# Kernel tuning notes

Hardware: AMD Instinct MI355X
Metric: run time of the kernel (lower is better)

## Reference

```python
import jax, jax.numpy as jnp
import numpy as np

D_MODEL = 1024
N_HEADS = 16
D_HEAD = D_MODEL // N_HEADS


def setup_inputs() -> dict:
    key = jax.random.key(0)
    k1, k2, k3 = jax.random.split(key, 3)
    B, T = 2, 2048
    x = jax.random.normal(k1, (B, T, D_MODEL), dtype=jnp.float32)
    key_padding_mask = jnp.zeros((B, T), dtype=bool)  # True = padded key
    # nn.Linear weights: [out_features, in_features], bias=False
    W_qkv = jax.random.normal(k2, (3 * D_MODEL, D_MODEL), dtype=jnp.float32) * (D_MODEL ** -0.5)
    W_proj = jax.random.normal(k3, (D_MODEL, D_MODEL), dtype=jnp.float32) * (D_MODEL ** -0.5)
    return {"x": x, "key_padding_mask": key_padding_mask, "W_qkv": W_qkv, "W_proj": W_proj}


def reference(x, key_padding_mask, W_qkv, W_proj):
    B, T, D = x.shape
    H, Dh = N_HEADS, D_HEAD
    scale = Dh ** -0.5
    # qkv: [B,T,3D] -> [3,B,H,T,Dh]
    qkv = (x @ W_qkv.T).reshape(B, T, 3, H, Dh).transpose(2, 0, 3, 1, 4)
    q, k, v = qkv[0], qkv[1], qkv[2]
    # attention scores [B,H,T,T]
    attn = jnp.einsum("bhqd,bhkd->bhqk", q, k) * scale
    attn = jnp.where(key_padding_mask[:, None, None, :], -jnp.inf, attn)
    attn = jax.nn.softmax(attn, axis=-1)  # dropout in eval mode = identity
    out = jnp.einsum("bhqk,bhkd->bhqd", attn, v)
    out = out.transpose(0, 2, 1, 3).reshape(B, T, D)
    return out @ W_proj.T
```

## Files before the change

### kernel.cpp

```cpp
#include <hip/hip_runtime.h>
#include <hip/hip_bf16.h>

typedef unsigned short u16;
typedef unsigned int u32;
typedef __bf16 bf16x8 __attribute__((ext_vector_type(8)));
typedef float f32x4 __attribute__((ext_vector_type(4)));

#define DMODEL 1024
#define NH 16
#define DH 64
#define BB 2
#define TT 2048
#define MM 4096
#define NQKV 3072
#define KVB 64

#define QSCALE 0.18033688011112042f

static __device__ __forceinline__ u16 f2bf(float f) {
  u32 u = __float_as_uint(f);
  u = (u + 0x7FFFu + ((u >> 16) & 1u)) >> 16;
  return (u16)u;
}

static __device__ __forceinline__ u32 pk2bf(float a, float b) {
  u16 ua = __builtin_bit_cast(u16, (__bf16)a);
  u16 ub = __builtin_bit_cast(u16, (__bf16)b);
  return (u32)ua | ((u32)ub << 16);
}

static __device__ __forceinline__ float fexp2(float x) {
#if __has_builtin(__builtin_amdgcn_exp2f)
  return __builtin_amdgcn_exp2f(x);
#else
  float r; asm("v_exp_f32 %0, %1" : "=v"(r) : "v"(x)); return r;
#endif
}

static __device__ __forceinline__ float max3f(float a, float b, float c) {
  return fmaxf(fmaxf(a, b), c);
}

static __device__ __forceinline__ void gload16(const u16* g, u16* l) {
  __builtin_amdgcn_global_load_lds(
      (const __attribute__((address_space(1))) void*)g,
      (__attribute__((address_space(3))) void*)l, 16, 0, 0);
}

#define N4X  (MM * DMODEL / 4)
#define N4W  (NQKV * DMODEL / 4)
#define N4P  (DMODEL * DMODEL / 4)
__global__ __launch_bounds__(256) void cvt_all(const float* __restrict__ x,
                                               const float* __restrict__ wqkv,
                                               const float* __restrict__ wproj,
                                               u16* __restrict__ dst) {
  int i = blockIdx.x * 256 + threadIdx.x;
  const float* src;
  int j = i;
  if (i < N4X) {
    src = x;
  } else if (i < N4X + N4W) {
    src = wqkv; j = i - N4X;
  } else {
    src = wproj; j = i - (N4X + N4W);
  }
  float4 v = reinterpret_cast<const float4*>(src)[j];
  ushort4 o;
  o.x = f2bf(v.x); o.y = f2bf(v.y); o.z = f2bf(v.z); o.w = f2bf(v.w);
  reinterpret_cast<ushort4*>(dst)[i] = o;
}

static __device__ __forceinline__ void gemm_stage(
    const u16* __restrict__ A, const u16* __restrict__ B, u16* As, u16* Bs,
    int r0, int o0, int r1, int o1, int c0, int c1, int kcol) {
  gload16(A + (size_t)r0 * DMODEL + kcol + o0, As + c0 * 8);
  gload16(A + (size_t)r1 * DMODEL + kcol + o1, As + c1 * 8);
  gload16(B + (size_t)r0 * DMODEL + kcol + o0, Bs + c0 * 8);
  gload16(B + (size_t)r1 * DMODEL + kcol + o1, Bs + c1 * 8);
}

static __device__ __forceinline__ void gemm128_mainloop(
    const u16* __restrict__ Abase, const u16* __restrict__ Bbase,
    u16* As, u16* Bs, f32x4 (&acc)[4][4]) {
  const int tid = threadIdx.x;
  const int lane = tid & 63;
  const int w = tid >> 6;
  const int rowg = lane >> 4, col = lane & 15;
  const int wm = w >> 1, wn = w & 1;
  const int c0 = tid, c1 = tid + 256;
  const int r0 = c0 >> 2, o0 = (c0 & 3) * 8;
  const int r1 = c1 >> 2, o1 = (c1 & 3) * 8;

  gemm_stage(Abase, Bbase, As, Bs, r0, o0, r1, o1, c0, c1, 0);
  asm volatile("s_waitcnt vmcnt(0)" ::: "memory");
  __builtin_amdgcn_s_barrier();

  int sel = 0;
  for (int kt = 0; kt < DMODEL / 32; ++kt) {
    const int kn = ((kt + 1) & (DMODEL / 32 - 1)) * 32;
    const int ns = sel ^ 1;
    gemm_stage(Abase, Bbase, As + ns * 4096, Bs + ns * 4096, r0, o0, r1, o1, c0, c1, kn);
    const u16* as = As + sel * 4096;
    const u16* bs = Bs + sel * 4096;
    bf16x8 af[4], bfr[4];
#pragma unroll
    for (int i = 0; i < 4; ++i)
      af[i] = *reinterpret_cast<const bf16x8*>(as + (wm * 64 + i * 16 + col) * 32 + rowg * 8);
#pragma unroll
    for (int j = 0; j < 4; ++j)
      bfr[j] = *reinterpret_cast<const bf16x8*>(bs + (wn * 64 + j * 16 + col) * 32 + rowg * 8);
#pragma unroll
    for (int i = 0; i < 4; ++i)
#pragma unroll
      for (int j = 0; j < 4; ++j)
        acc[i][j] = __builtin_amdgcn_mfma_f32_16x16x32_bf16(af[i], bfr[j], acc[i][j], 0, 0, 0);
    asm volatile("s_waitcnt vmcnt(0)" ::: "memory");
    __builtin_amdgcn_s_barrier();
    sel = ns;
  }
}

__global__ __launch_bounds__(256, 3) void qkv_gemm(
    const u16* __restrict__ xb, const u16* __restrict__ wb,
    u16* __restrict__ qb, u16* __restrict__ kb, u16* __restrict__ vtb) {
  __shared__ u16 As[2 * 128 * 32];
  __shared__ u16 Bs[2 * 128 * 32];
  f32x4 acc[4][4];
#pragma unroll
  for (int i = 0; i < 4; ++i)
#pragma unroll
    for (int j = 0; j < 4; ++j) acc[i][j] = (f32x4){0.f, 0.f, 0.f, 0.f};
  gemm128_mainloop(xb + (size_t)blockIdx.y * 128 * DMODEL,
                   wb + (size_t)blockIdx.x * 128 * DMODEL, As, Bs, acc);
  const int lane = threadIdx.x & 63, w = threadIdx.x >> 6;
  const int rowg = lane >> 4, col = lane & 15, wm = w >> 1, wn = w & 1;
#pragma unroll
  for (int i = 0; i < 4; ++i) {
#pragma unroll
    for (int j = 0; j < 4; ++j) {
#pragma unroll
      for (int r = 0; r < 4; ++r) {
        int m = blockIdx.y * 128 + wm * 64 + i * 16 + rowg * 4 + r;
        int n = blockIdx.x * 128 + wn * 64 + j * 16 + col;
        int b = m >> 11, t = m & (TT - 1);
        int s = n >> 10, h = (n >> 6) & 15, d = n & 63;
        int bh = b * NH + h;
        float v = acc[i][j][r];
        if (s == 0)      qb[((size_t)bh * TT + t) * DH + d] = f2bf(v * QSCALE);
        else if (s == 1) kb[((size_t)bh * TT + t) * DH + d] = f2bf(v);
        else             vtb[((size_t)bh * DH + d) * TT + t] = f2bf(v);
      }
    }
  }
}

__global__ __launch_bounds__(256, 3) void proj_gemm(
    const u16* __restrict__ ab, const u16* __restrict__ wb, float* __restrict__ out) {
  __shared__ u16 As[2 * 128 * 32];
  __shared__ u16 Bs[2 * 128 * 32];
  f32x4 acc[4][4];
#pragma unroll
  for (int i = 0; i < 4; ++i)
#pragma unroll
    for (int j = 0; j < 4; ++j) acc[i][j] = (f32x4){0.f, 0.f, 0.f, 0.f};
  gemm128_mainloop(ab + (size_t)blockIdx.y * 128 * DMODEL,
                   wb + (size_t)blockIdx.x * 128 * DMODEL, As, Bs, acc);
  const int lane = threadIdx.x & 63, w = threadIdx.x >> 6;
  const int rowg = lane >> 4, col = lane & 15, wm = w >> 1, wn = w & 1;
#pragma unroll
  for (int i = 0; i < 4; ++i) {
#pragma unroll
    for (int j = 0; j < 4; ++j) {
#pragma unroll
      for (int r = 0; r < 4; ++r) {
        int m = blockIdx.y * 128 + wm * 64 + i * 16 + rowg * 4 + r;
        int n = blockIdx.x * 128 + wn * 64 + j * 16 + col;
        out[(size_t)m * DMODEL + n] = acc[i][j][r];
      }
    }
  }
}

static __device__ __forceinline__ void attn_stage(
    const u16* __restrict__ kbase, const u16* __restrict__ vbase,
    int kt, u16* KsSel, u16* VsSel, int tid) {
  int row = tid >> 3;
  int bI = (tid & 7) * 16;
  gload16(kbase + kt * (KVB * DH) + row * DH + ((bI ^ ((row & 7) << 4)) >> 1), KsSel + tid * 8);
  gload16(vbase + (size_t)row * TT + kt * KVB + ((bI ^ ((row & 7) << 4)) >> 1), VsSel + tid * 8);
}

__global__ __launch_bounds__(512, 2) void attn_kernel(
    const u16* __restrict__ qb, const u16* __restrict__ kb,
    const u16* __restrict__ vtb, const unsigned char* __restrict__ mask,
    u16* __restrict__ ob) {
  __shared__ u16 Ks[2][KVB * DH];
  __shared__ u16 Vs[2][DH * KVB];
  __shared__ u16 Pl[8][16 * KVB];
  __shared__ unsigned char maskb[TT];
  __shared__ u32 mflag;

  const int tid = threadIdx.x;
  const int lane = tid & 63, w = tid >> 6;
  const int rowg = lane >> 4, col = lane & 15;
  const int qt = blockIdx.x, bh = blockIdx.y;
  const int b = bh >> 4;

  if (tid == 0) mflag = 0;
  __syncthreads();

  {
    u32 m0 = reinterpret_cast<const u32*>(mask + (size_t)b * TT)[tid];
    *reinterpret_cast<u32*>(maskb + tid * 4) = m0;
    if (m0) atomicOr(&mflag, 1u << (tid >> 4));
  }

  const int qrow0 = qt * 128 + w * 16;
  const u16* qptr = qb + ((size_t)bh * TT + qrow0) * DH;
  bf16x8 a_q[2];
#pragma unroll
  for (int ds = 0; ds < 2; ++ds)
    a_q[ds] = *reinterpret_cast<const bf16x8*>(qptr + col * DH + ds * 32 + rowg * 8);

  f32x4 acc_o[4];
  float m_run = -1e30f, l_run = 0.f;
#pragma unroll
  for (int df = 0; df < 4; ++df) acc_o[df] = (f32x4){0.f, 0.f, 0.f, 0.f};

  const u16* kbase = kb + (size_t)bh * TT * DH;
  const u16* vbase = vtb + (size_t)bh * DH * TT;
  u16* pw = Pl[w];

  attn_stage(kbase, vbase, 0, Ks[0], Vs[0], tid);
  __syncthreads();
  const u32 fm = mflag;

  int cur = 0;
  for (int t = 0; t < TT / KVB; ++t) {
    const int tn = (t + 1) & (TT / KVB - 1);
    attn_stage(kbase, vbase, tn, Ks[cur ^ 1], Vs[cur ^ 1], tid);

    f32x4 sc[4];
#pragma unroll
    for (int kf = 0; kf < 4; ++kf) sc[kf] = (f32x4){0.f, 0.f, 0.f, 0.f};
    const u16* ks = Ks[cur];
#pragma unroll
    for (int ds = 0; ds < 2; ++ds) {
      bf16x8 ak[4];
#pragma unroll
      for (int kf = 0; kf < 4; ++kf) {
        int krow = kf * 16 + col;
        ak[kf] = *reinterpret_cast<const bf16x8*>(
            ks + krow * DH + (((ds * 64 + rowg * 16) ^ ((krow & 7) << 4)) >> 1));
      }
#pragma unroll
      for (int kf = 0; kf < 4; ++kf)
        sc[kf] = __builtin_amdgcn_mfma_f32_16x16x32_bf16(ak[kf], a_q[ds], sc[kf], 0, 0, 0);
    }

    if (fm & (1u << t)) {
#pragma unroll
      for (int kf = 0; kf < 4; ++kf)
#pragma unroll
        for (int r = 0; r < 4; ++r)
          sc[kf][r] += maskb[t * KVB + kf * 16 + rowg * 4 + r] ? -1e30f : 0.f;
    }

    {
      float t0 = max3f(sc[0][0], sc[0][1], sc[0][2]);
      float t1 = max3f(sc[0][3], sc[1][0], sc[1][1]);
      float t2 = max3f(sc[1][2], sc[1][3], sc[2][0]);
      float t3 = max3f(sc[2][1], sc[2][2], sc[2][3]);
      float t4 = max3f(sc[3][0], sc[3][1], sc[3][2]);
      float mx = fmaxf(max3f(t0, t1, t2), max3f(t3, t4, sc[3][3]));
      mx = fmaxf(mx, __shfl_xor(mx, 16, 64));
      mx = fmaxf(mx, __shfl_xor(mx, 32, 64));
      if (__any(mx > m_run + 8.0f)) {
        float mn = fmaxf(m_run, mx);
        float corr = fexp2(m_run - mn);
        m_run = mn;
        l_run *= corr;
#pragma unroll
        for (int df = 0; df < 4; ++df) acc_o[df] *= corr;
      }
      const float mc = m_run;

      const int sw = (col & 7) << 4;
      u16* prow = pw + col * KVB;
      float rs = 0.f;
#pragma unroll
      for (int kf = 0; kf < 4; ++kf) {
        float p0 = fexp2(sc[kf][0] - mc);
        float p1 = fexp2(sc[kf][1] - mc);
        float p2 = fexp2(sc[kf][2] - mc);
        float p3 = fexp2(sc[kf][3] - mc);
        rs += (p0 + p1) + (p2 + p3);
        uint2 pk;
        pk.x = pk2bf(p0, p1);
        pk.y = pk2bf(p2, p3);
        int bI = kf * 32 + rowg * 8;
        *reinterpret_cast<uint2*>(prow + ((bI ^ sw) >> 1)) = pk;
      }
      rs += __shfl_xor(rs, 16, 64);
      rs += __shfl_xor(rs, 32, 64);
      l_run += rs;
    }
    asm volatile("s_waitcnt lgkmcnt(0)" ::: "memory");
    __builtin_amdgcn_sched_barrier(0);

    const u16* vs = Vs[cur];
    __builtin_amdgcn_s_setprio(1);
#pragma unroll
    for (int ksI = 0; ksI < 2; ++ksI) {
      bf16x8 bp = *reinterpret_cast<const bf16x8*>(
          pw + col * KVB + (((ksI * 64 + rowg * 16) ^ ((col & 7) << 4)) >> 1));
#pragma unroll
      for (int df = 0; df < 4; ++df) {
        int vrow = df * 16 + col;
        bf16x8 bv = *reinterpret_cast<const bf16x8*>(
            vs + vrow * KVB + (((ksI * 64 + rowg * 16) ^ ((vrow & 7) << 4)) >> 1));
        acc_o[df] = __builtin_amdgcn_mfma_f32_16x16x32_bf16(bv, bp, acc_o[df], 0, 0, 0);
      }
    }
    __builtin_amdgcn_s_setprio(0);

    asm volatile("s_waitcnt vmcnt(0)" ::: "memory");
    __builtin_amdgcn_s_barrier();
    cur ^= 1;
  }

  const int h = bh & 15;
  {
    float inv = 1.f / l_run;
    int tq = qrow0 + col;
    size_t rowoff = ((size_t)(b * TT + tq)) * DMODEL + h * DH + rowg * 4;
#pragma unroll
    for (int df = 0; df < 4; ++df) {
      ushort4 o4;
      o4.x = f2bf(acc_o[df][0] * inv);
      o4.y = f2bf(acc_o[df][1] * inv);
      o4.z = f2bf(acc_o[df][2] * inv);
      o4.w = f2bf(acc_o[df][3] * inv);
      *reinterpret_cast<ushort4*>(ob + rowoff + df * 16) = o4;
    }
  }
}

extern "C" void kernel_launch(void* const* d_in, const int* in_sizes, int n_in,
                              void* d_out, int out_size, void* d_ws, size_t ws_size,
                              hipStream_t stream) {
  const float* x = (const float*)d_in[0];
  const unsigned char* mask = (const unsigned char*)d_in[1];
  const float* wqkv = (const float*)d_in[2];
  const float* wproj = (const float*)d_in[3];
  float* out = (float*)d_out;

  u16* xb     = (u16*)d_ws;
  u16* wqkvb  = xb    + (size_t)MM * DMODEL;
  u16* wprojb = wqkvb + (size_t)NQKV * DMODEL;
  u16* qb     = wprojb + (size_t)DMODEL * DMODEL;
  u16* kb     = qb + (size_t)MM * DMODEL;
  u16* vtb    = kb + (size_t)MM * DMODEL;
  u16* ob     = vtb + (size_t)MM * DMODEL;

  cvt_all<<<(N4X + N4W + N4P) / 256, 256, 0, stream>>>(x, wqkv, wproj, xb);
  qkv_gemm<<<dim3(NQKV / 128, MM / 128), 256, 0, stream>>>(xb, wqkvb, qb, kb, vtb);
  attn_kernel<<<dim3(TT / 128, BB * NH), 512, 0, stream>>>(qb, kb, vtb, mask, ob);
  proj_gemm<<<dim3(DMODEL / 128, MM / 128), 256, 0, stream>>>(ob, wprojb, out);
}
```

Baseline: 135.1 us.

## Switch attention to 32x32x16 MFMA with register-resident P via permlane32 swap

Restructures the attention kernel into 4 waves of 32 query rows each, using 32x32x16 bf16 MFMAs instead of 16x16x32. The softmax probabilities now stay in registers and are rearranged with v_permlane32_swap into the B-operand layout, removing the per-wave P round trip through LDS and its waitcnt. The block drops from 512 to 256 threads, each thread loads two K/V chunks, and the output is staged through swizzled LDS so global stores are coalesced 16-byte writes. The cost is more registers per thread and fewer waves per block, which may lower latency hiding.

```diff
diff --git a/kernel.cpp b/kernel.cpp
--- a/kernel.cpp
+++ b/kernel.cpp
@@ -5,6 +5,7 @@
 typedef unsigned int u32;
 typedef __bf16 bf16x8 __attribute__((ext_vector_type(8)));
 typedef float f32x4 __attribute__((ext_vector_type(4)));
+typedef float f32x16 __attribute__((ext_vector_type(16)));
 
 #define DMODEL 1024
 #define NH 16
@@ -184,25 +185,33 @@
 static __device__ __forceinline__ void attn_stage(
     const u16* __restrict__ kbase, const u16* __restrict__ vbase,
     int kt, u16* KsSel, u16* VsSel, int tid) {
-  int row = tid >> 3;
-  int bI = (tid & 7) * 16;
-  gload16(kbase + kt * (KVB * DH) + row * DH + ((bI ^ ((row & 7) << 4)) >> 1), KsSel + tid * 8);
-  gload16(vbase + (size_t)row * TT + kt * KVB + ((bI ^ ((row & 7) << 4)) >> 1), VsSel + tid * 8);
-}
-
-__global__ __launch_bounds__(512, 2) void attn_kernel(
+#pragma unroll
+  for (int p = 0; p < 2; ++p) {
+    int c = p * 256 + tid;
+    int row = c >> 3;
+    int bI = (c & 7) * 16;
+    gload16(kbase + kt * (KVB * DH) + row * DH + ((bI ^ ((row & 7) << 4)) >> 1), KsSel + c * 8);
+  }
+#pragma unroll
+  for (int p = 0; p < 2; ++p) {
+    int c = p * 256 + tid;
+    int d = c >> 3;
+    int bI = (c & 7) * 16;
+    gload16(vbase + (size_t)d * TT + kt * KVB + ((bI ^ ((d & 7) << 4)) >> 1), VsSel + c * 8);
+  }
+}
+
+__global__ __launch_bounds__(256, 2) void attn_kernel(
     const u16* __restrict__ qb, const u16* __restrict__ kb,
     const u16* __restrict__ vtb, const unsigned char* __restrict__ mask,
     u16* __restrict__ ob) {
-  __shared__ u16 Ks[2][KVB * DH];
-  __shared__ u16 Vs[2][DH * KVB];
-  __shared__ u16 Pl[8][16 * KVB];
+  __shared__ u16 SM[2][2][KVB * DH];
   __shared__ unsigned char maskb[TT];
   __shared__ u32 mflag;
 
   const int tid = threadIdx.x;
   const int lane = tid & 63, w = tid >> 6;
-  const int rowg = lane >> 4, col = lane & 15;
+  const int col = lane & 31, h = lane >> 5;
   const int qt = blockIdx.x, bh = blockIdx.y;
   const int b = bh >> 4;
 
@@ -210,70 +219,85 @@
   __syncthreads();
 
   {
-    u32 m0 = reinterpret_cast<const u32*>(mask + (size_t)b * TT)[tid];
-    *reinterpret_cast<u32*>(maskb + tid * 4) = m0;
-    if (m0) atomicOr(&mflag, 1u << (tid >> 4));
-  }
-
-  const int qrow0 = qt * 128 + w * 16;
+    const u32* mg = reinterpret_cast<const u32*>(mask + (size_t)b * TT);
+    u32 m0 = mg[tid * 2], m1 = mg[tid * 2 + 1];
+    *reinterpret_cast<u32*>(maskb + tid * 8) = m0;
+    *reinterpret_cast<u32*>(maskb + tid * 8 + 4) = m1;
+    if (m0 | m1) atomicOr(&mflag, 1u << (tid >> 3));
+  }
+
+  const int qrow0 = qt * 128 + w * 32;
   const u16* qptr = qb + ((size_t)bh * TT + qrow0) * DH;
-  bf16x8 a_q[2];
-#pragma unroll
-  for (int ds = 0; ds < 2; ++ds)
-    a_q[ds] = *reinterpret_cast<const bf16x8*>(qptr + col * DH + ds * 32 + rowg * 8);
-
-  f32x4 acc_o[4];
+  bf16x8 aq[4];
+#pragma unroll
+  for (int dstep = 0; dstep < 4; ++dstep)
+    aq[dstep] = *reinterpret_cast<const bf16x8*>(qptr + col * DH + dstep * 16 + h * 8);
+
+  f32x16 acc[2];
+#pragma unroll
+  for (int df = 0; df < 2; ++df)
+#pragma unroll
+    for (int r = 0; r < 16; ++r) acc[df][r] = 0.f;
   float m_run = -1e30f, l_run = 0.f;
-#pragma unroll
-  for (int df = 0; df < 4; ++df) acc_o[df] = (f32x4){0.f, 0.f, 0.f, 0.f};
 
   const u16* kbase = kb + (size_t)bh * TT * DH;
   const u16* vbase = vtb + (size_t)bh * DH * TT;
-  u16* pw = Pl[w];
-
-  attn_stage(kbase, vbase, 0, Ks[0], Vs[0], tid);
+
+  attn_stage(kbase, vbase, 0, SM[0][0], SM[0][1], tid);
   __syncthreads();
   const u32 fm = mflag;
 
   int cur = 0;
   for (int t = 0; t < TT / KVB; ++t) {
     const int tn = (t + 1) & (TT / KVB - 1);
-    attn_stage(kbase, vbase, tn, Ks[cur ^ 1], Vs[cur ^ 1], tid);
-
-    f32x4 sc[4];
-#pragma unroll
-    for (int kf = 0; kf < 4; ++kf) sc[kf] = (f32x4){0.f, 0.f, 0.f, 0.f};
-    const u16* ks = Ks[cur];
-#pragma unroll
-    for (int ds = 0; ds < 2; ++ds) {
-      bf16x8 ak[4];
-#pragma unroll
-      for (int kf = 0; kf < 4; ++kf) {
-        int krow = kf * 16 + col;
+    attn_stage(kbase, vbase, tn, SM[cur ^ 1][0], SM[cur ^ 1][1], tid);
+
+    const u16* ks = SM[cur][0];
+    const u16* vs = SM[cur][1];
+
+    f32x16 sc[2];
+#pragma unroll
+    for (int kf = 0; kf < 2; ++kf)
+#pragma unroll
+      for (int r = 0; r < 16; ++r) sc[kf][r] = 0.f;
+#pragma unroll
+    for (int dstep = 0; dstep < 4; ++dstep) {
+      bf16x8 ak[2];
+#pragma unroll
+      for (int kf = 0; kf < 2; ++kf) {
+        int row = kf * 32 + col;
         ak[kf] = *reinterpret_cast<const bf16x8*>(
-            ks + krow * DH + (((ds * 64 + rowg * 16) ^ ((krow & 7) << 4)) >> 1));
-      }
-#pragma unroll
-      for (int kf = 0; kf < 4; ++kf)
-        sc[kf] = __builtin_amdgcn_mfma_f32_16x16x32_bf16(ak[kf], a_q[ds], sc[kf], 0, 0, 0);
+            ks + row * DH + (((dstep * 32 + h * 16) ^ ((row & 7) << 4)) >> 1));
+      }
+#pragma unroll
+      for (int kf = 0; kf < 2; ++kf)
+        sc[kf] = __builtin_amdgcn_mfma_f32_32x32x16_bf16(ak[kf], aq[dstep], sc[kf], 0, 0, 0);
     }
 
     if (fm & (1u << t)) {
 #pragma unroll
-      for (int kf = 0; kf < 4; ++kf)
-#pragma unroll
-        for (int r = 0; r < 4; ++r)
-          sc[kf][r] += maskb[t * KVB + kf * 16 + rowg * 4 + r] ? -1e30f : 0.f;
+      for (int kf = 0; kf < 2; ++kf)
+#pragma unroll
+        for (int r = 0; r < 16; ++r) {
+          int key = kf * 32 + (r & 3) + 8 * (r >> 2) + 4 * h;
+          sc[kf][r] += maskb[t * KVB + key] ? -1e30f : 0.f;
+        }
     }
 
     {
       float t0 = max3f(sc[0][0], sc[0][1], sc[0][2]);
-      float t1 = max3f(sc[0][3], sc[1][0], sc[1][1]);
-      float t2 = max3f(sc[1][2], sc[1][3], sc[2][0]);
-      float t3 = max3f(sc[2][1], sc[2][2], sc[2][3]);
-      float t4 = max3f(sc[3][0], sc[3][1], sc[3][2]);
-      float mx = fmaxf(max3f(t0, t1, t2), max3f(t3, t4, sc[3][3]));
-      mx = fmaxf(mx, __shfl_xor(mx, 16, 64));
+      float t1 = max3f(sc[0][3], sc[0][4], sc[0][5]);
+      float t2 = max3f(sc[0][6], sc[0][7], sc[0][8]);
+      float t3 = max3f(sc[0][9], sc[0][10], sc[0][11]);
+      float t4 = max3f(sc[0][12], sc[0][13], sc[0][14]);
+      float t5 = max3f(sc[0][15], sc[1][0], sc[1][1]);
+      float t6 = max3f(sc[1][2], sc[1][3], sc[1][4]);
+      float t7 = max3f(sc[1][5], sc[1][6], sc[1][7]);
+      float t8 = max3f(sc[1][8], sc[1][9], sc[1][10]);
+      float t9 = max3f(sc[1][11], sc[1][12], sc[1][13]);
+      float ta = fmaxf(sc[1][14], sc[1][15]);
+      float mx = fmaxf(max3f(max3f(t0, t1, t2), max3f(t3, t4, t5), max3f(t6, t7, t8)),
+                       max3f(t9, ta, -1e30f));
       mx = fmaxf(mx, __shfl_xor(mx, 32, 64));
       if (__any(mx > m_run + 8.0f)) {
         float mn = fmaxf(m_run, mx);
@@ -281,45 +305,48 @@
         m_run = mn;
         l_run *= corr;
 #pragma unroll
-        for (int df = 0; df < 4; ++df) acc_o[df] *= corr;
+        for (int df = 0; df < 2; ++df)
+#pragma unroll
+          for (int r = 0; r < 16; ++r) acc[df][r] *= corr;
       }
       const float mc = m_run;
-
-      const int sw = (col & 7) << 4;
-      u16* prow = pw + col * KVB;
       float rs = 0.f;
 #pragma unroll
-      for (int kf = 0; kf < 4; ++kf) {
-        float p0 = fexp2(sc[kf][0] - mc);
-        float p1 = fexp2(sc[kf][1] - mc);
-        float p2 = fexp2(sc[kf][2] - mc);
-        float p3 = fexp2(sc[kf][3] - mc);
-        rs += (p0 + p1) + (p2 + p3);
-        uint2 pk;
-        pk.x = pk2bf(p0, p1);
-        pk.y = pk2bf(p2, p3);
-        int bI = kf * 32 + rowg * 8;
-        *reinterpret_cast<uint2*>(prow + ((bI ^ sw) >> 1)) = pk;
-      }
-      rs += __shfl_xor(rs, 16, 64);
+      for (int kf = 0; kf < 2; ++kf)
+#pragma unroll
+        for (int r = 0; r < 16; ++r) {
+          float p = fexp2(sc[kf][r] - mc);
+          sc[kf][r] = p;
+          rs += p;
+        }
       rs += __shfl_xor(rs, 32, 64);
       l_run += rs;
     }
-    asm volatile("s_waitcnt lgkmcnt(0)" ::: "memory");
-    __builtin_amdgcn_sched_barrier(0);
-
-    const u16* vs = Vs[cur];
+
+    u32 P2[2][8];
+#pragma unroll
+    for (int kf = 0; kf < 2; ++kf)
+#pragma unroll
+      for (int i = 0; i < 8; ++i)
+        P2[kf][i] = pk2bf(sc[kf][2 * i], sc[kf][2 * i + 1]);
+
     __builtin_amdgcn_s_setprio(1);
 #pragma unroll
-    for (int ksI = 0; ksI < 2; ++ksI) {
-      bf16x8 bp = *reinterpret_cast<const bf16x8*>(
-          pw + col * KVB + (((ksI * 64 + rowg * 16) ^ ((col & 7) << 4)) >> 1));
-#pragma unroll
-      for (int df = 0; df < 4; ++df) {
-        int vrow = df * 16 + col;
-        bf16x8 bv = *reinterpret_cast<const bf16x8*>(
-            vs + vrow * KVB + (((ksI * 64 + rowg * 16) ^ ((vrow & 7) << 4)) >> 1));
-        acc_o[df] = __builtin_amdgcn_mfma_f32_16x16x32_bf16(bv, bp, acc_o[df], 0, 0, 0);
+    for (int ksl = 0; ksl < 4; ++ksl) {
+      const int kf = ksl >> 1;
+      const int i0 = (ksl & 1) * 4;
+      u32 w0 = P2[kf][i0],     w2 = P2[kf][i0 + 2];
+      u32 w1 = P2[kf][i0 + 1], w3 = P2[kf][i0 + 3];
+      asm("v_permlane32_swap_b32 %0, %1" : "+v"(w0), "+v"(w2));
+      asm("v_permlane32_swap_b32 %0, %1" : "+v"(w1), "+v"(w3));
+      u32 bpw[4] = {w0, w1, w2, w3};
+      bf16x8 bp = __builtin_bit_cast(bf16x8, *reinterpret_cast<uint4*>(bpw));
+#pragma unroll
+      for (int df = 0; df < 2; ++df) {
+        int row = df * 32 + col;
+        bf16x8 av = *reinterpret_cast<const bf16x8*>(
+            vs + row * KVB + (((ksl * 32 + h * 16) ^ ((row & 7) << 4)) >> 1));
+        acc[df] = __builtin_amdgcn_mfma_f32_32x32x16_bf16(av, bp, acc[df], 0, 0, 0);
       }
     }
     __builtin_amdgcn_s_setprio(0);
@@ -329,19 +356,36 @@
     cur ^= 1;
   }
 
-  const int h = bh & 15;
+  u16* Ol = &SM[0][0][0];
   {
     float inv = 1.f / l_run;
-    int tq = qrow0 + col;
-    size_t rowoff = ((size_t)(b * TT + tq)) * DMODEL + h * DH + rowg * 4;
-#pragma unroll
-    for (int df = 0; df < 4; ++df) {
-      ushort4 o4;
-      o4.x = f2bf(acc_o[df][0] * inv);
-      o4.y = f2bf(acc_o[df][1] * inv);
-      o4.z = f2bf(acc_o[df][2] * inv);
-      o4.w = f2bf(acc_o[df][3] * inv);
-      *reinterpret_cast<ushort4*>(ob + rowoff + df * 16) = o4;
+    const int q = w * 32 + col;
+    const int swzq = (q ^ (q >> 3)) & 7;
+#pragma unroll
+    for (int df = 0; df < 2; ++df) {
+#pragma unroll
+      for (int a = 0; a < 4; ++a) {
+        uint2 pk;
+        pk.x = pk2bf(acc[df][4 * a] * inv, acc[df][4 * a + 1] * inv);
+        pk.y = pk2bf(acc[df][4 * a + 2] * inv, acc[df][4 * a + 3] * inv);
+        int d2 = df * 64 + a * 16 + h * 8;
+        int byte = q * 128 + (d2 ^ (swzq << 4));
+        *reinterpret_cast<uint2*>(reinterpret_cast<char*>(Ol) + byte) = pk;
+      }
+    }
+  }
+  __syncthreads();
+  {
+    const int hh = bh & 15;
+#pragma unroll
+    for (int p = 0; p < 4; ++p) {
+      int idx = p * 256 + tid;
+      int q = idx >> 3, ch = idx & 7;
+      int swzq = (q ^ (q >> 3)) & 7;
+      uint4 v = *reinterpret_cast<const uint4*>(
+          reinterpret_cast<const char*>(Ol) + q * 128 + ((ch * 16) ^ (swzq << 4)));
+      size_t row = (size_t)(b * TT + qt * 128 + q);
+      *reinterpret_cast<uint4*>(ob + row * DMODEL + hh * DH + ch * 8) = v;
     }
   }
 }
@@ -365,6 +409,6 @@
 
   cvt_all<<<(N4X + N4W + N4P) / 256, 256, 0, stream>>>(x, wqkv, wproj, xb);
   qkv_gemm<<<dim3(NQKV / 128, MM / 128), 256, 0, stream>>>(xb, wqkvb, qb, kb, vtb);
-  attn_kernel<<<dim3(TT / 128, BB * NH), 512, 0, stream>>>(qb, kb, vtb, mask, ob);
+  attn_kernel<<<dim3(TT / 128, BB * NH), 256, 0, stream>>>(qb, kb, vtb, mask, ob);
   proj_gemm<<<dim3(DMODEL / 128, MM / 128), 256, 0, stream>>>(ob, wprojb, out);
 }
```

New measurement: 135.3 us. About the same (+0.1%).
